# Kernel tuning notes

Hardware: AMD Instinct MI355X
Metric: run time of the kernel (lower is better)

Reference implementation:

```python
import jax, jax.numpy as jnp
import numpy as np

B = 96            # batch; must equal out_features for the rank-growing matmul broadcast to type-check
IN_FEATURES = 3
OUT_FEATURES = 96
GRID_PLUS_ORDER = 5 + 3  # grid_size + spline_order


def setup_inputs() -> dict:
    key = jax.random.key(0)
    k1, k2 = jax.random.split(key)
    x = jax.random.normal(k1, (B, IN_FEATURES), dtype=jnp.float32)
    spline_weight = jax.random.normal(k2, (OUT_FEATURES, IN_FEATURES, GRID_PLUS_ORDER), dtype=jnp.float32)
    return {"x": x, "spline_weight": spline_weight}


def reference(x, spline_weight):
    # projected[b, o, j] = sum_i x[b, i] * W[o, i, j]  -> [B, out, G+k]
    projected = jnp.einsum('bi,oij->boj', x, spline_weight)
    res = projected[:, :, 0]  # [B, out]
    # Non-commutative composition: each step is an outer-product-style matmul that
    # grows the rank by one 'out' dim (numpy matmul broadcasting == torch's here).
    for i in range(1, IN_FEATURES):
        res = jnp.squeeze(jnp.matmul(res[..., None], projected[:, :, i][:, None, :]))
    return res  # [B, out, out, out] for in_features=3 with B == out
```

## Files before the change

kernel.cpp:

```cpp
#include <hip/hip_runtime.h>


#define NB 96
#define TBL (NB * NB)

typedef float f32x4 __attribute__((ext_vector_type(4)));

__global__ __launch_bounds__(256) void prep_kernel(
    const float* __restrict__ x,
    const float* __restrict__ w,
    float* __restrict__ ws)
{
    const int v = blockIdx.x * 256 + threadIdx.x;
    if (v >= 3 * TBL) return;
    const int which = v / TBL;
    const int r     = v % TBL;
    const int a     = r / NB;
    const int c     = r % NB;
    const float x0 = x[a*3 + 0], x1 = x[a*3 + 1], x2 = x[a*3 + 2];
    const int j = which;
    ws[v] = x0 * w[c*24 + 0*8 + j] + x1 * w[c*24 + 1*8 + j] + x2 * w[c*24 + 2*8 + j];
}

__global__ __launch_bounds__(256) void nckart_store(
    const float* __restrict__ ws,
    float* __restrict__ out)
{
    const int bm = blockIdx.x;
    const int b  = bm / NB;
    const int m  = bm % NB;
    const int t  = threadIdx.x;

    const float*  s  = ws;
    const float*  p1 = ws + TBL;
    const f32x4*  q4 = reinterpret_cast<const f32x4*>(ws + 2 * TBL);

    const float A = s[bm];
    f32x4* o4 = reinterpret_cast<f32x4*>(out) + (size_t)bm * (NB * NB / 4);

    #pragma unroll
    for (int it = 0; it < 9; ++it) {
        const int idx = t + it * 256;
        const int n   = idx / 24;
        const int p4  = idx % 24;
        f32x4 v = q4[m * 24 + p4];
        v *= (A * p1[b * NB + n]);
        o4[idx] = v;
    }
}

extern "C" void kernel_launch(void* const* d_in, const int* in_sizes, int n_in,
                              void* d_out, int out_size, void* d_ws, size_t ws_size,
                              hipStream_t stream) {
    const float* x = (const float*)d_in[0];
    const float* w = (const float*)d_in[1];
    float* out = (float*)d_out;
    float* ws  = (float*)d_ws;

    prep_kernel<<<(3 * TBL + 255) / 256, 256, 0, stream>>>(x, w, ws);
    nckart_store<<<TBL, 256, 0, stream>>>(ws, out);
}
```

Before: 69.49 us.

## Replace per-(b,m) blocks with grid-stride sweep over flat output

```diff
diff --git a/kernel.cpp b/kernel.cpp
--- a/kernel.cpp
+++ b/kernel.cpp
@@ -3,6 +3,10 @@
 
 #define NB 96
 #define TBL (NB * NB)
+#define TOT4 (TBL * TBL / 4)
+#define NBLK 2048
+#define NTHR (NBLK * 256)
+#define NIT ((TOT4 + NTHR - 1) / NTHR)
 
 typedef float f32x4 __attribute__((ext_vector_type(4)));
 
@@ -18,34 +22,34 @@
     const int a     = r / NB;
     const int c     = r % NB;
     const float x0 = x[a*3 + 0], x1 = x[a*3 + 1], x2 = x[a*3 + 2];
-    const int j = which;
-    ws[v] = x0 * w[c*24 + 0*8 + j] + x1 * w[c*24 + 1*8 + j] + x2 * w[c*24 + 2*8 + j];
+    ws[v] = x0 * w[c*24 + which] + x1 * w[c*24 + 8 + which] + x2 * w[c*24 + 16 + which];
 }
 
-__global__ __launch_bounds__(256) void nckart_store(
+__global__ __launch_bounds__(256) void nckart_sweep(
     const float* __restrict__ ws,
     float* __restrict__ out)
 {
-    const int bm = blockIdx.x;
-    const int b  = bm / NB;
-    const int m  = bm % NB;
-    const int t  = threadIdx.x;
+    const int t = blockIdx.x * 256 + threadIdx.x;
 
-    const float*  s  = ws;
-    const float*  p1 = ws + TBL;
-    const f32x4*  q4 = reinterpret_cast<const f32x4*>(ws + 2 * TBL);
-
-    const float A = s[bm];
-    f32x4* o4 = reinterpret_cast<f32x4*>(out) + (size_t)bm * (NB * NB / 4);
+    const float* s  = ws;
+    const float* p1 = ws + TBL;
+    const f32x4* q4 = reinterpret_cast<const f32x4*>(ws + 2 * TBL);
+    f32x4* o4 = reinterpret_cast<f32x4*>(out);
 
     #pragma unroll
-    for (int it = 0; it < 9; ++it) {
-        const int idx = t + it * 256;
-        const int n   = idx / 24;
-        const int p4  = idx % 24;
-        f32x4 v = q4[m * 24 + p4];
-        v *= (A * p1[b * NB + n]);
-        o4[idx] = v;
+    for (int it = 0; it < NIT; ++it) {
+        const unsigned idx = (unsigned)t + (unsigned)it * NTHR;
+        if (idx < TOT4) {
+            const unsigned row = idx / 24u;
+            const unsigned p4  = idx - row * 24u;
+            const unsigned bm  = row / 96u;
+            const unsigned n   = row - bm * 96u;
+            const unsigned b   = bm / 96u;
+            const unsigned m   = bm - b * 96u;
+            f32x4 v = q4[m * 24u + p4];
+            v *= s[bm] * p1[b * 96u + n];
+            o4[idx] = v;
+        }
     }
 }
 
@@ -58,5 +62,5 @@
     float* ws  = (float*)d_ws;
 
     prep_kernel<<<(3 * TBL + 255) / 256, 256, 0, stream>>>(x, w, ws);
-    nckart_store<<<TBL, 256, 0, stream>>>(ws, out);
+    nckart_sweep<<<NBLK, 256, 0, stream>>>(ws, out);
 }
```

After: 72.06 us. 1.04x slower.
